# Performance work log

Hardware: AMD Instinct MI355X
Metric: run time of the kernel (lower is better)

The kernel has to match this reference:

```python
import jax, jax.numpy as jnp
import numpy as np

B, T, C, H = 4, 4096, 1024, 128

def setup_inputs() -> dict:
    key = jax.random.key(0)
    k1, k2, k3, k4 = jax.random.split(key, 4)
    x = jax.random.normal(k1, (B, T, C), dtype=jnp.float32)
    # nn.Linear(embed, head, bias=False): y = x @ W, store W as [C, H]
    s = 1.0 / np.sqrt(C)
    Wk = jax.random.normal(k2, (C, H), dtype=jnp.float32) * s
    Wq = jax.random.normal(k3, (C, H), dtype=jnp.float32) * s
    Wv = jax.random.normal(k4, (C, H), dtype=jnp.float32) * s
    return {"x": x, "Wk": Wk, "Wq": Wq, "Wv": Wv}

def reference(x, Wk, Wq, Wv):
    Bx, Tx, Cx = x.shape
    scale = Wk.shape[1] ** -0.5
    k = x @ Wk  # [B,T,H]
    q = x @ Wq
    v = x @ Wv
    att = jnp.einsum('bth,bsh->bts', q, k) * scale  # [B,T,T]
    causal = jnp.triu(jnp.ones((Tx, Tx), dtype=bool), k=1)
    att = jnp.where(causal, -jnp.inf, att)
    att = jax.nn.softmax(att, axis=-1)
    # dropout is identity in eval mode
    out = jnp.einsum('bts,bsh->bth', att, v)  # [B,T,H]
    return out
```

## Files before the change

kernel.cpp:

```cpp
#include <hip/hip_runtime.h>
#include <stdint.h>
#include <math.h>

#define B_ 4
#define T_ 4096
#define C_ 1024
#define H_ 128

typedef __attribute__((ext_vector_type(8))) short s16x8;
typedef __attribute__((ext_vector_type(4))) float f32x4;

__device__ __forceinline__ unsigned short f2bf(float f) {
    union { float f; unsigned u; } v; v.f = f;
    unsigned r = v.u + 0x7fffu + ((v.u >> 16) & 1u);
    return (unsigned short)(r >> 16);
}

__device__ __forceinline__ s16x8 as_frag(uint4 u) {
    union { uint4 u; s16x8 s; } v; v.u = u; return v.s;
}

__host__ __device__ constexpr int chunks_total(int CH) {
    int a = 64 / CH, b = 64 % CH;
    return CH * a * (a + 1) / 2 + b * (a + 1);
}

#define QSC (0.0883883476f * 1.4426950408f)

__global__ __launch_bounds__(256) void k_wt(const float* __restrict__ Wk,
                                            const float* __restrict__ Wq,
                                            const float* __restrict__ Wv,
                                            unsigned short* __restrict__ Wt) {
    __shared__ float tile[64][65];
    int w = blockIdx.z;
    const float* W = (w == 0) ? Wk : (w == 1) ? Wq : Wv;
    int c0 = blockIdx.x * 64, h0 = blockIdx.y * 64;
    int tid = threadIdx.x;
#pragma unroll
    for (int k = 0; k < 16; k++) {
        int idx = tid + k * 256;
        int r = idx >> 6, c = idx & 63;
        tile[r][c] = W[(size_t)(c0 + r) * H_ + h0 + c];
    }
    __syncthreads();
#pragma unroll
    for (int k = 0; k < 16; k++) {
        int idx = tid + k * 256;
        int hh = idx >> 6, cc = idx & 63;
        Wt[(size_t)(w * H_ + h0 + hh) * C_ + c0 + cc] = f2bf(tile[cc][hh]);
    }
}

__global__ __launch_bounds__(256, 3) void k_qkv(const float* __restrict__ x,
                                                const unsigned short* __restrict__ Wt,
                                                unsigned short* __restrict__ Qb,
                                                unsigned short* __restrict__ Kb,
                                                unsigned short* __restrict__ Vt) {
    __shared__ unsigned short a_lds[2][64 * 72];
    int tid = threadIdx.x;
    int wv = tid >> 6, lane = tid & 63, quad = lane >> 4, lo = lane & 15;
    int r0 = blockIdx.x * 64;
    int cb = blockIdx.y;
    int nt0 = wv * 3;

    f32x4 acc[3][4];
#pragma unroll
    for (int i = 0; i < 3; i++)
#pragma unroll
        for (int j = 0; j < 4; j++) acc[i][j] = (f32x4){0.f, 0.f, 0.f, 0.f};

    const int row_s = tid >> 2;
    const int seg_s = (tid & 3) * 16;
    size_t xbase = (size_t)(r0 + row_s) * C_ + seg_s;

    const unsigned short* wp[3];
#pragma unroll
    for (int nt = 0; nt < 3; nt++)
        wp[nt] = Wt + (size_t)(cb * 192 + (nt0 + nt) * 16 + lo) * C_ + quad * 8;

    auto pack_store = [&](unsigned short* buf, const float4 (&f)[4]) {
        uint4 u0, u1;
        u0.x = (unsigned)f2bf(f[0].x) | ((unsigned)f2bf(f[0].y) << 16);
        u0.y = (unsigned)f2bf(f[0].z) | ((unsigned)f2bf(f[0].w) << 16);
        u0.z = (unsigned)f2bf(f[1].x) | ((unsigned)f2bf(f[1].y) << 16);
        u0.w = (unsigned)f2bf(f[1].z) | ((unsigned)f2bf(f[1].w) << 16);
        u1.x = (unsigned)f2bf(f[2].x) | ((unsigned)f2bf(f[2].y) << 16);
        u1.y = (unsigned)f2bf(f[2].z) | ((unsigned)f2bf(f[2].w) << 16);
        u1.z = (unsigned)f2bf(f[3].x) | ((unsigned)f2bf(f[3].y) << 16);
        u1.w = (unsigned)f2bf(f[3].z) | ((unsigned)f2bf(f[3].w) << 16);
        *(uint4*)&buf[row_s * 72 + seg_s] = u0;
        *(uint4*)&buf[row_s * 72 + seg_s + 8] = u1;
    };
    auto load_x = [&](float4 (&f)[4], int kc) {
        const float* xp = x + xbase + kc * 64;
#pragma unroll
        for (int j = 0; j < 4; j++) f[j] = *(const float4*)(xp + j * 4);
    };

    float4 xr[4];
    load_x(xr, 0);
    pack_store(a_lds[0], xr);
    __syncthreads();

    for (int kc = 0; kc < 16; kc++) {
        const unsigned short* buf = a_lds[kc & 1];
        float4 xn[4];
        if (kc < 15) load_x(xn, kc + 1);
        s16x8 b[3][2];
#pragma unroll
        for (int nt = 0; nt < 3; nt++)
#pragma unroll
            for (int kh = 0; kh < 2; kh++)
                b[nt][kh] = *(const s16x8*)(wp[nt] + kc * 64 + kh * 32);
        s16x8 af[4][2];
#pragma unroll
        for (int mt = 0; mt < 4; mt++)
#pragma unroll
            for (int kh = 0; kh < 2; kh++)
                af[mt][kh] = *(const s16x8*)&buf[(mt * 16 + lo) * 72 + kh * 32 + quad * 8];
#pragma unroll
        for (int nt = 0; nt < 3; nt++)
#pragma unroll
            for (int kh = 0; kh < 2; kh++)
#pragma unroll
                for (int mt = 0; mt < 4; mt++)
                    acc[nt][mt] = __builtin_amdgcn_mfma_f32_16x16x32_bf16(
                        af[mt][kh], b[nt][kh], acc[nt][mt], 0, 0, 0);
        if (kc < 15) pack_store((unsigned short*)a_lds[(kc & 1) ^ 1], xn);
        __syncthreads();
    }

#pragma unroll
    for (int nt = 0; nt < 3; nt++) {
        int col = cb * 192 + (nt0 + nt) * 16 + lo;
        int w = col >> 7, h = col & 127;
#pragma unroll
        for (int mt = 0; mt < 4; mt++) {
            int mrow = r0 + mt * 16 + quad * 4;
            if (w == 2) {
                int b = mrow >> 12, t0 = mrow & 4095;
                int tp = (t0 & ~31) + (((t0 & 15) >> 2) << 3) + (((t0 >> 4) & 1) << 2);
                uint2 pk;
                pk.x = (unsigned)f2bf(acc[nt][mt][0]) | ((unsigned)f2bf(acc[nt][mt][1]) << 16);
                pk.y = (unsigned)f2bf(acc[nt][mt][2]) | ((unsigned)f2bf(acc[nt][mt][3]) << 16);
                *(uint2*)(Vt + (size_t)(b * H_ + h) * T_ + tp) = pk;
            } else if (w == 1) {
                unsigned short* dst = Qb + (size_t)mrow * H_ + h;
#pragma unroll
                for (int r = 0; r < 4; r++)
                    dst[(size_t)r * H_] = f2bf(acc[nt][mt][r] * QSC);
            } else {
                unsigned short* dst = Kb + (size_t)mrow * H_ + h;
#pragma unroll
                for (int r = 0; r < 4; r++)
                    dst[(size_t)r * H_] = f2bf(acc[nt][mt][r]);
            }
        }
    }
}

#define LOAD_KV(kv0)                                                            \
    do {                                                                        \
        const uint4* kg = (const uint4*)(Kb + (size_t)(batch * T_ + (kv0) + srow_k) * H_); \
        pk0 = kg[sseg_k + 0]; pk1 = kg[sseg_k + 1];                             \
        pk2 = kg[sseg_k + 2]; pk3 = kg[sseg_k + 3];                             \
        const uint4* vg = (const uint4*)(Vt + (size_t)(batch * H_ + srow_v) * T_ + (kv0)); \
        pv0 = vg[sseg_v + 0]; pv1 = vg[sseg_v + 1];                             \
        pv2 = vg[sseg_v + 2]; pv3 = vg[sseg_v + 3];                             \
    } while (0)

template <int CH>
__global__ __launch_bounds__(256, 4) void k_attn(const unsigned short* __restrict__ Qb,
                                                 const unsigned short* __restrict__ Kb,
                                                 const unsigned short* __restrict__ Vt,
                                                 float* __restrict__ Opart,
                                                 float* __restrict__ Mpart,
                                                 float* __restrict__ Lpart,
                                                 float* __restrict__ out) {
    __shared__ uint4 kbuf[64 * 16];
    __shared__ uint4 vbuf[128 * 8];

    int tid = threadIdx.x;
    int wv = tid >> 6, lane = tid & 63, quad = lane >> 4, lo = lane & 15;

    int id = blockIdx.x;
    int qt, batch, tbeg, tend, slot = 0;
    if constexpr (CH > 0) {
        int e = id & 1;
        batch = (id >> 1) & 3;
        int g = id >> 3;
        slot = g * 2 + e;
        int s = slot, q = 63;
        for (;;) { int nc = (q + CH) / CH; if (s < nc) break; s -= nc; --q; }
        qt = q;
        tbeg = s * CH;
        tend = min(tbeg + CH, qt + 1);
    } else {
        qt = 63 - (id >> 2); batch = id & 3;
        tbeg = 0; tend = qt + 1;
    }
    int m0 = qt * 64 + wv * 16;
    int query = m0 + lo;

    s16x8 qf[4];
    size_t qrow = (size_t)(batch * T_ + m0 + lo) * H_;
#pragma unroll
    for (int ks = 0; ks < 4; ks++)
        qf[ks] = *(const s16x8*)(Qb + qrow + ks * 32 + quad * 8);

    f32x4 acc_o[8];
#pragma unroll
    for (int o = 0; o < 8; o++) acc_o[o] = (f32x4){0.f, 0.f, 0.f, 0.f};
    float m_i = -INFINITY, l_i = 0.f;

    const int srow_k = tid >> 2, sseg_k = (tid & 3) * 4;
    const int srow_v = tid >> 1, sseg_v = (tid & 1) * 4;

    uint4 pk0, pk1, pk2, pk3, pv0, pv1, pv2, pv3;
    LOAD_KV(tbeg * 64);

    for (int t = tbeg; t < tend; ++t) {
        int kv0 = t * 64;
        kbuf[srow_k * 16 + ((sseg_k + 0) ^ (srow_k & 15))] = pk0;
        kbuf[srow_k * 16 + ((sseg_k + 1) ^ (srow_k & 15))] = pk1;
        kbuf[srow_k * 16 + ((sseg_k + 2) ^ (srow_k & 15))] = pk2;
        kbuf[srow_k * 16 + ((sseg_k + 3) ^ (srow_k & 15))] = pk3;
        vbuf[srow_v * 8 + ((sseg_v + 0) ^ (srow_v & 7))] = pv0;
        vbuf[srow_v * 8 + ((sseg_v + 1) ^ (srow_v & 7))] = pv1;
        vbuf[srow_v * 8 + ((sseg_v + 2) ^ (srow_v & 7))] = pv2;
        vbuf[srow_v * 8 + ((sseg_v + 3) ^ (srow_v & 7))] = pv3;
        __syncthreads();
        if (t + 1 < tend) LOAD_KV((t + 1) * 64);

        f32x4 s_acc[4];
#pragma unroll
        for (int nt = 0; nt < 4; nt++) s_acc[nt] = (f32x4){0.f, 0.f, 0.f, 0.f};
        __builtin_amdgcn_s_setprio(1);
#pragma unroll
        for (int ks = 0; ks < 4; ks++) {
#pragma unroll
            for (int nt = 0; nt < 4; nt++) {
                s16x8 kf = as_frag(kbuf[(nt * 16 + lo) * 16 + ((ks * 4 + quad) ^ lo)]);
                s_acc[nt] = __builtin_amdgcn_mfma_f32_16x16x32_bf16(kf, qf[ks], s_acc[nt], 0, 0, 0);
            }
        }
        __builtin_amdgcn_s_setprio(0);

        float p[4][4];
#pragma unroll
        for (int nt = 0; nt < 4; nt++)
#pragma unroll
            for (int r = 0; r < 4; r++) p[nt][r] = s_acc[nt][r];
        if (t == qt) {
#pragma unroll
            for (int nt = 0; nt < 4; nt++)
#pragma unroll
                for (int r = 0; r < 4; r++)
                    if (kv0 + nt * 16 + quad * 4 + r > query) p[nt][r] = -INFINITY;
        }

        float mx = p[0][0];
#pragma unroll
        for (int nt = 0; nt < 4; nt++)
#pragma unroll
            for (int r = 0; r < 4; r++) mx = fmaxf(mx, p[nt][r]);
        if (__any(mx > m_i + 8.0f)) {
            float rm = fmaxf(mx, __shfl_xor(mx, 16));
            rm = fmaxf(rm, __shfl_xor(rm, 32));
            float mnew = fmaxf(m_i, rm);
            float alpha = exp2f(m_i - mnew);
            l_i *= alpha;
            m_i = mnew;
#pragma unroll
            for (int o = 0; o < 8; o++)
#pragma unroll
                for (int r = 0; r < 4; r++) acc_o[o][r] *= alpha;
        }
        float rs = 0.f;
#pragma unroll
        for (int nt = 0; nt < 4; nt++)
#pragma unroll
            for (int r = 0; r < 4; r++) {
                float pv = exp2f(p[nt][r] - m_i);
                p[nt][r] = pv;
                rs += pv;
            }
        l_i += rs;

        s16x8 pf[2];
#pragma unroll
        for (int kt = 0; kt < 2; kt++) {
            uint4 u;
            u.x = (__float_as_uint(p[2 * kt][0]) >> 16) | ((__float_as_uint(p[2 * kt][1]) >> 16) << 16);
            u.y = (__float_as_uint(p[2 * kt][2]) >> 16) | ((__float_as_uint(p[2 * kt][3]) >> 16) << 16);
            u.z = (__float_as_uint(p[2 * kt + 1][0]) >> 16) | ((__float_as_uint(p[2 * kt + 1][1]) >> 16) << 16);
            u.w = (__float_as_uint(p[2 * kt + 1][2]) >> 16) | ((__float_as_uint(p[2 * kt + 1][3]) >> 16) << 16);
            pf[kt] = as_frag(u);
        }

        __builtin_amdgcn_s_setprio(1);
#pragma unroll
        for (int kt = 0; kt < 2; kt++)
#pragma unroll
            for (int o = 0; o < 8; o++) {
                int vrow = o * 16 + lo;
                s16x8 vf = as_frag(vbuf[vrow * 8 + ((kt * 4 + quad) ^ (vrow & 7))]);
                acc_o[o] = __builtin_amdgcn_mfma_f32_16x16x32_bf16(vf, pf[kt], acc_o[o], 0, 0, 0);
            }
        __builtin_amdgcn_s_setprio(0);
        __syncthreads();
    }

    l_i += __shfl_xor(l_i, 16);
    l_i += __shfl_xor(l_i, 32);

    if constexpr (CH > 0) {
        constexpr int NCH = chunks_total(CH);
        size_t pr = (size_t)(batch * NCH + slot) * 64 + wv * 16 + lo;
        float* Op = Opart + pr * 128;
#pragma unroll
        for (int o = 0; o < 8; o++)
            __builtin_nontemporal_store(acc_o[o], (f32x4*)(Op + o * 16 + quad * 4));
        if (quad == 0) { Mpart[pr] = m_i; Lpart[pr] = l_i; }
    } else {
        float inv = 1.0f / l_i;
        int rowg = batch * T_ + m0 + lo;
#pragma unroll
        for (int o = 0; o < 8; o++) {
            f32x4 v = {acc_o[o][0] * inv, acc_o[o][1] * inv,
                       acc_o[o][2] * inv, acc_o[o][3] * inv};
            __builtin_nontemporal_store(v, (f32x4*)(out + (size_t)rowg * H_ + o * 16 + quad * 4));
        }
    }
}

template <int CH>
__global__ __launch_bounds__(256) void k_comb(const float* __restrict__ Opart,
                                              const float* __restrict__ Mpart,
                                              const float* __restrict__ Lpart,
                                              float* __restrict__ out) {
    constexpr int NCH = chunks_total(CH);
    int tid = threadIdx.x;
    int row = blockIdx.x * 8 + (tid >> 5);
    int h4 = (tid & 31) * 4;
    int batch = row >> 12, t = row & 4095, qt = t >> 6;
    int n = qt + 1;
    int nc = (qt + CH) / CH;
    int a = n / CH, b = n % CH;
    int S = CH * a * (a + 1) / 2 + b * (a + 1);
    int base = NCH - S;
    float M = -INFINITY, den = 0.f;
    float4 o = {0.f, 0.f, 0.f, 0.f};
    for (int s = 0; s < nc; ++s) {
        size_t pr = (size_t)(batch * NCH + base + s) * 64 + (t & 63);
        float ms = Mpart[pr], ls = Lpart[pr];
        float4 v = *(const float4*)(Opart + pr * 128 + h4);
        float Mn = fmaxf(M, ms);
        float wa = exp2f(M - Mn), wb = exp2f(ms - Mn);
        den = den * wa + ls * wb;
        o.x = o.x * wa + v.x * wb;
        o.y = o.y * wa + v.y * wb;
        o.z = o.z * wa + v.z * wb;
        o.w = o.w * wa + v.w * wb;
        M = Mn;
    }
    float inv = 1.0f / den;
    float4 r = {o.x * inv, o.y * inv, o.z * inv, o.w * inv};
    *(float4*)(out + (size_t)row * H_ + h4) = r;
}

extern "C" void kernel_launch(void* const* d_in, const int* in_sizes, int n_in,
                              void* d_out, int out_size, void* d_ws, size_t ws_size,
                              hipStream_t stream) {
    const float* x  = (const float*)d_in[0];
    const float* Wk = (const float*)d_in[1];
    const float* Wq = (const float*)d_in[2];
    const float* Wv = (const float*)d_in[3];
    char* ws = (char*)d_ws;
    unsigned short* Wt = (unsigned short*)ws;
    unsigned short* Qb = (unsigned short*)(ws + (1u << 20));
    unsigned short* Kb = (unsigned short*)(ws + (5u << 20));
    unsigned short* Vt = (unsigned short*)(ws + (9u << 20));
    float* out = (float*)d_out;

    const size_t base = (size_t)13 << 20;
    constexpr int NCH10 = chunks_total(10);
    constexpr int NCH21 = chunks_total(21);
    static_assert(NCH10 % 2 == 0 && NCH21 % 2 == 0, "XCD decode needs even NCH");
    auto need_for = [&](int nch) {
        return base + (size_t)4 * nch * 64 * (128 * 4) + 2 * (size_t)4 * nch * 64 * 4;
    };

    k_wt  <<<dim3(16, 2, 3), 256, 0, stream>>>(Wk, Wq, Wv, Wt);
    k_qkv <<<dim3(256, 2), 256, 0, stream>>>(x, Wt, Qb, Kb, Vt);

    if (ws_size >= need_for(NCH10)) {
        float* Op = (float*)(ws + base);
        float* Mp = Op + (size_t)4 * NCH10 * 64 * 128;
        float* Lp = Mp + (size_t)4 * NCH10 * 64;
        k_attn<10><<<4 * NCH10, 256, 0, stream>>>(Qb, Kb, Vt, Op, Mp, Lp, out);
        k_comb<10><<<2048, 256, 0, stream>>>(Op, Mp, Lp, out);
    } else if (ws_size >= need_for(NCH21)) {
        float* Op = (float*)(ws + base);
        float* Mp = Op + (size_t)4 * NCH21 * 64 * 128;
        float* Lp = Mp + (size_t)4 * NCH21 * 64;
        k_attn<21><<<4 * NCH21, 256, 0, stream>>>(Qb, Kb, Vt, Op, Mp, Lp, out);
        k_comb<21><<<2048, 256, 0, stream>>>(Op, Mp, Lp, out);
    } else {
        k_attn<0><<<256, 256, 0, stream>>>(Qb, Kb, Vt, nullptr, nullptr, nullptr, out);
    }
}
```

Measured before the change: 173.0 us.

## Use 128-row query blocks with 8 waves sharing each K/V tile

The attention kernel now handles 128 query rows per block with 512 threads (8 waves), so each K/V tile staged in shared memory serves twice as many queries. The per-thread global loads are halved, the split-KV chunk decode and combine indexing are reworked for 128-row blocks, and the default chunk size drops to 6 tiles. The causal mask now tests per wave against the KV range. This cuts redundant K/V traffic but gives fewer, larger blocks, which may worsen load balance and occupancy, and the non-split fallback path is removed.

```diff
diff --git a/kernel.cpp b/kernel.cpp
--- a/kernel.cpp
+++ b/kernel.cpp
@@ -20,9 +20,10 @@
     union { uint4 u; s16x8 s; } v; v.u = u; return v.s;
 }
 
-__host__ __device__ constexpr int chunks_total(int CH) {
-    int a = 64 / CH, b = 64 % CH;
-    return CH * a * (a + 1) / 2 + b * (a + 1);
+__host__ __device__ constexpr int chunks128(int CH) {
+    int H2 = CH / 2;
+    int k = 32 / H2, r = 32 % H2;
+    return H2 * k * (k + 1) / 2 + r * (k + 1);
 }
 
 #define QSC (0.0883883476f * 1.4426950408f)
@@ -163,20 +164,17 @@
     do {                                                                        \
         const uint4* kg = (const uint4*)(Kb + (size_t)(batch * T_ + (kv0) + srow_k) * H_); \
         pk0 = kg[sseg_k + 0]; pk1 = kg[sseg_k + 1];                             \
-        pk2 = kg[sseg_k + 2]; pk3 = kg[sseg_k + 3];                             \
         const uint4* vg = (const uint4*)(Vt + (size_t)(batch * H_ + srow_v) * T_ + (kv0)); \
         pv0 = vg[sseg_v + 0]; pv1 = vg[sseg_v + 1];                             \
-        pv2 = vg[sseg_v + 2]; pv3 = vg[sseg_v + 3];                             \
     } while (0)
 
 template <int CH>
-__global__ __launch_bounds__(256, 4) void k_attn(const unsigned short* __restrict__ Qb,
+__global__ __launch_bounds__(512, 6) void k_attn(const unsigned short* __restrict__ Qb,
                                                  const unsigned short* __restrict__ Kb,
                                                  const unsigned short* __restrict__ Vt,
                                                  float* __restrict__ Opart,
                                                  float* __restrict__ Mpart,
-                                                 float* __restrict__ Lpart,
-                                                 float* __restrict__ out) {
+                                                 float* __restrict__ Lpart) {
     __shared__ uint4 kbuf[64 * 16];
     __shared__ uint4 vbuf[128 * 8];
 
@@ -184,22 +182,14 @@
     int wv = tid >> 6, lane = tid & 63, quad = lane >> 4, lo = lane & 15;
 
     int id = blockIdx.x;
-    int qt, batch, tbeg, tend, slot = 0;
-    if constexpr (CH > 0) {
-        int e = id & 1;
-        batch = (id >> 1) & 3;
-        int g = id >> 3;
-        slot = g * 2 + e;
-        int s = slot, q = 63;
-        for (;;) { int nc = (q + CH) / CH; if (s < nc) break; s -= nc; --q; }
-        qt = q;
-        tbeg = s * CH;
-        tend = min(tbeg + CH, qt + 1);
-    } else {
-        qt = 63 - (id >> 2); batch = id & 3;
-        tbeg = 0; tend = qt + 1;
-    }
-    int m0 = qt * 64 + wv * 16;
+    int batch = id & 3;
+    int slot = id >> 2;
+    int s = slot, q = 31;
+    for (;;) { int nc = (2 * q + 1 + CH) / CH; if (s < nc) break; s -= nc; --q; }
+    int qb = q;
+    int tbeg = s * CH;
+    int tend = min(tbeg + CH, 2 * qb + 2);
+    int m0 = qb * 128 + wv * 16;
     int query = m0 + lo;
 
     s16x8 qf[4];
@@ -213,22 +203,18 @@
     for (int o = 0; o < 8; o++) acc_o[o] = (f32x4){0.f, 0.f, 0.f, 0.f};
     float m_i = -INFINITY, l_i = 0.f;
 
-    const int srow_k = tid >> 2, sseg_k = (tid & 3) * 4;
-    const int srow_v = tid >> 1, sseg_v = (tid & 1) * 4;
-
-    uint4 pk0, pk1, pk2, pk3, pv0, pv1, pv2, pv3;
+    const int srow_k = tid >> 3, sseg_k = (tid & 7) * 2;
+    const int srow_v = tid >> 2, sseg_v = (tid & 3) * 2;
+
+    uint4 pk0, pk1, pv0, pv1;
     LOAD_KV(tbeg * 64);
 
     for (int t = tbeg; t < tend; ++t) {
         int kv0 = t * 64;
         kbuf[srow_k * 16 + ((sseg_k + 0) ^ (srow_k & 15))] = pk0;
         kbuf[srow_k * 16 + ((sseg_k + 1) ^ (srow_k & 15))] = pk1;
-        kbuf[srow_k * 16 + ((sseg_k + 2) ^ (srow_k & 15))] = pk2;
-        kbuf[srow_k * 16 + ((sseg_k + 3) ^ (srow_k & 15))] = pk3;
         vbuf[srow_v * 8 + ((sseg_v + 0) ^ (srow_v & 7))] = pv0;
         vbuf[srow_v * 8 + ((sseg_v + 1) ^ (srow_v & 7))] = pv1;
-        vbuf[srow_v * 8 + ((sseg_v + 2) ^ (srow_v & 7))] = pv2;
-        vbuf[srow_v * 8 + ((sseg_v + 3) ^ (srow_v & 7))] = pv3;
         __syncthreads();
         if (t + 1 < tend) LOAD_KV((t + 1) * 64);
 
@@ -251,7 +237,7 @@
         for (int nt = 0; nt < 4; nt++)
 #pragma unroll
             for (int r = 0; r < 4; r++) p[nt][r] = s_acc[nt][r];
-        if (t == qt) {
+        if (kv0 + 63 > m0) {
 #pragma unroll
             for (int nt = 0; nt < 4; nt++)
 #pragma unroll
@@ -314,24 +300,15 @@
     l_i += __shfl_xor(l_i, 16);
     l_i += __shfl_xor(l_i, 32);
 
-    if constexpr (CH > 0) {
-        constexpr int NCH = chunks_total(CH);
-        size_t pr = (size_t)(batch * NCH + slot) * 64 + wv * 16 + lo;
-        float* Op = Opart + pr * 128;
-#pragma unroll
-        for (int o = 0; o < 8; o++)
-            __builtin_nontemporal_store(acc_o[o], (f32x4*)(Op + o * 16 + quad * 4));
-        if (quad == 0) { Mpart[pr] = m_i; Lpart[pr] = l_i; }
-    } else {
-        float inv = 1.0f / l_i;
-        int rowg = batch * T_ + m0 + lo;
-#pragma unroll
-        for (int o = 0; o < 8; o++) {
-            f32x4 v = {acc_o[o][0] * inv, acc_o[o][1] * inv,
-                       acc_o[o][2] * inv, acc_o[o][3] * inv};
-            __builtin_nontemporal_store(v, (f32x4*)(out + (size_t)rowg * H_ + o * 16 + quad * 4));
-        }
-    }
+    constexpr int NCH = chunks128(CH);
+    size_t pr = (size_t)(batch * NCH + slot) * 128 + wv * 16 + lo;
+    float* Op = Opart + pr * 128;
+#pragma unroll
+    for (int o = 0; o < 8; o++) {
+        float4 v = {acc_o[o][0], acc_o[o][1], acc_o[o][2], acc_o[o][3]};
+        *(float4*)(Op + o * 16 + quad * 4) = v;
+    }
+    if (quad == 0) { Mpart[pr] = m_i; Lpart[pr] = l_i; }
 }
 
 template <int CH>
@@ -339,20 +316,20 @@
                                               const float* __restrict__ Mpart,
                                               const float* __restrict__ Lpart,
                                               float* __restrict__ out) {
-    constexpr int NCH = chunks_total(CH);
+    constexpr int NCH = chunks128(CH);
+    constexpr int H2 = CH / 2;
     int tid = threadIdx.x;
     int row = blockIdx.x * 8 + (tid >> 5);
     int h4 = (tid & 31) * 4;
-    int batch = row >> 12, t = row & 4095, qt = t >> 6;
-    int n = qt + 1;
-    int nc = (qt + CH) / CH;
-    int a = n / CH, b = n % CH;
-    int S = CH * a * (a + 1) / 2 + b * (a + 1);
-    int base = NCH - S;
+    int batch = row >> 12, t = row & 4095, qb = t >> 7, rr = t & 127;
+    int nc = (2 * qb + 1 + CH) / CH;
+    int n = qb + 1, k = n / H2, r = n % H2;
+    int F = H2 * k * (k + 1) / 2 + r * (k + 1);
+    int base = NCH - F;
     float M = -INFINITY, den = 0.f;
     float4 o = {0.f, 0.f, 0.f, 0.f};
     for (int s = 0; s < nc; ++s) {
-        size_t pr = (size_t)(batch * NCH + base + s) * 64 + (t & 63);
+        size_t pr = (size_t)(batch * NCH + base + s) * 128 + rr;
         float ms = Mpart[pr], ls = Lpart[pr];
         float4 v = *(const float4*)(Opart + pr * 128 + h4);
         float Mn = fmaxf(M, ms);
@@ -365,8 +342,8 @@
         M = Mn;
     }
     float inv = 1.0f / den;
-    float4 r = {o.x * inv, o.y * inv, o.z * inv, o.w * inv};
-    *(float4*)(out + (size_t)row * H_ + h4) = r;
+    float4 rz = {o.x * inv, o.y * inv, o.z * inv, o.w * inv};
+    *(float4*)(out + (size_t)row * H_ + h4) = rz;
 }
 
 extern "C" void kernel_launch(void* const* d_in, const int* in_sizes, int n_in,
@@ -384,29 +361,26 @@
     float* out = (float*)d_out;
 
     const size_t base = (size_t)13 << 20;
-    constexpr int NCH10 = chunks_total(10);
-    constexpr int NCH21 = chunks_total(21);
-    static_assert(NCH10 % 2 == 0 && NCH21 % 2 == 0, "XCD decode needs even NCH");
+    constexpr int N6  = chunks128(6);
+    constexpr int N10 = chunks128(10);
     auto need_for = [&](int nch) {
-        return base + (size_t)4 * nch * 64 * (128 * 4) + 2 * (size_t)4 * nch * 64 * 4;
+        return base + (size_t)4 * nch * 128 * (128 * 4) + 2 * (size_t)4 * nch * 128 * 4;
     };
 
     k_wt  <<<dim3(16, 2, 3), 256, 0, stream>>>(Wk, Wq, Wv, Wt);
     k_qkv <<<dim3(256, 2), 256, 0, stream>>>(x, Wt, Qb, Kb, Vt);
 
-    if (ws_size >= need_for(NCH10)) {
+    if (ws_size >= need_for(N6)) {
         float* Op = (float*)(ws + base);
-        float* Mp = Op + (size_t)4 * NCH10 * 64 * 128;
-        float* Lp = Mp + (size_t)4 * NCH10 * 64;
-        k_attn<10><<<4 * NCH10, 256, 0, stream>>>(Qb, Kb, Vt, Op, Mp, Lp, out);
+        float* Mp = Op + (size_t)4 * N6 * 128 * 128;
+        float* Lp = Mp + (size_t)4 * N6 * 128;
+        k_attn<6><<<4 * N6, 512, 0, stream>>>(Qb, Kb, Vt, Op, Mp, Lp);
+        k_comb<6><<<2048, 256, 0, stream>>>(Op, Mp, Lp, out);
+    } else {
+        float* Op = (float*)(ws + base);
+        float* Mp = Op + (size_t)4 * N10 * 128 * 128;
+        float* Lp = Mp + (size_t)4 * N10 * 128;
+        k_attn<10><<<4 * N10, 512, 0, stream>>>(Qb, Kb, Vt, Op, Mp, Lp);
         k_comb<10><<<2048, 256, 0, stream>>>(Op, Mp, Lp, out);
-    } else if (ws_size >= need_for(NCH21)) {
-        float* Op = (float*)(ws + base);
-        float* Mp = Op + (size_t)4 * NCH21 * 64 * 128;
-        float* Lp = Mp + (size_t)4 * NCH21 * 64;
-        k_attn<21><<<4 * NCH21, 256, 0, stream>>>(Qb, Kb, Vt, Op, Mp, Lp, out);
-        k_comb<21><<<2048, 256, 0, stream>>>(Op, Mp, Lp, out);
-    } else {
-        k_attn<0><<<256, 256, 0, stream>>>(Qb, Kb, Vt, nullptr, nullptr, nullptr, out);
-    }
-}
+    }
+}
```

Result: slower. 231.2 us (+33.6%).
